# Kernel tuning notes

Hardware: AMD Instinct MI355X
Metric: run time of the kernel (lower is better)

The kernel has to match this reference:

```python
import jax, jax.numpy as jnp
import numpy as np

EMB = 300
H = 1024
V = 50004  # tgt_vocab_size + 4
B = 64
L = 1024


def setup_inputs() -> dict:
    key = jax.random.key(0)
    ks = jax.random.split(key, 16)
    s = 0.02
    return {
        "input": jax.random.randint(ks[0], (B,), 0, V),
        "hidden": jax.random.normal(ks[1], (1, B, H), jnp.float32),
        "source_hiddens": jax.random.normal(ks[2], (L, B, H), jnp.float32),
        "mask_src": jax.random.randint(ks[3], (B, L), 0, 2).astype(bool),
        "emb": jax.random.normal(ks[4], (V, EMB), jnp.float32) * s,
        "w_ih": jax.random.normal(ks[5], (3 * H, EMB), jnp.float32) * s,
        "w_hh": jax.random.normal(ks[6], (3 * H, H), jnp.float32) * s,
        "b_ih": jnp.zeros((3 * H,), jnp.float32),
        "b_hh": jnp.zeros((3 * H,), jnp.float32),
        "w_attn": jax.random.normal(ks[7], (H, H), jnp.float32) * s,
        "b_attn": jnp.zeros((H,), jnp.float32),
        "w_lin": jax.random.normal(ks[8], (H, 2 * H), jnp.float32) * s,
        "b_lin": jnp.zeros((H,), jnp.float32),
        "w_out": jax.random.normal(ks[9], (V, H), jnp.float32) * s,
        "b_out": jnp.zeros((V,), jnp.float32),
    }


def _decode_step(input, hidden, source_hiddens, mask_src, emb, w_ih, w_hh,
                 b_ih, b_hh, w_attn, b_attn, w_lin, b_lin, w_out, b_out):
    # Embedding lookup: [B, EMB]
    x = emb[input]
    h = hidden[0]  # [B, H]
    # GRU cell (PyTorch gate order: r, z, n)
    gi = x @ w_ih.T + b_ih          # [B, 3H]
    gh = h @ w_hh.T + b_hh          # [B, 3H]
    i_r, i_z, i_n = jnp.split(gi, 3, axis=-1)
    h_r, h_z, h_n = jnp.split(gh, 3, axis=-1)
    r = jax.nn.sigmoid(i_r + h_r)
    z = jax.nn.sigmoid(i_z + h_z)
    n = jnp.tanh(i_n + r * h_n)
    h_new = (1.0 - z) * n + z * h   # [B, H]

    # Bilinear attention over source: x_i' W y
    src = jnp.transpose(source_hiddens, (1, 0, 2))  # [B, L, H]
    Wy = h_new @ w_attn.T + b_attn                  # [B, H]
    xWy = jnp.einsum('blh,bh->bl', src, Wy)         # [B, L]
    xWy = jnp.where(mask_src, -jnp.inf, xWy)
    scores = jax.nn.softmax(xWy, axis=-1)           # [B, L]
    context = jnp.einsum('bl,blh->bh', scores, src) # [B, H]

    fused = jnp.tanh(jnp.concatenate([context, h_new], axis=1) @ w_lin.T + b_lin)
    logits = fused @ w_out.T + b_out                # [B, V]
    logp = jax.nn.log_softmax(logits, axis=1)
    return logp, h_new[None], scores


def reference(input, hidden, source_hiddens, mask_src, emb, w_ih, w_hh,
              b_ih, b_hh, w_attn, b_attn, w_lin, b_lin, w_out, b_out):
    return _decode_step(input, hidden, source_hiddens, mask_src, emb, w_ih,
                        w_hh, b_ih, b_hh, w_attn, b_attn, w_lin, b_lin,
                        w_out, b_out)
```

## Files before the change

### kernel.cpp

```cpp
#include <hip/hip_runtime.h>
#include <math.h>

#define EMB 300
#define HD  1024
#define VOC 50004
#define BB  64
#define LL  1024
#define NCH 16

typedef __attribute__((ext_vector_type(8))) short short8;
typedef __attribute__((ext_vector_type(4))) float f32x4;

#define WS_XT    0
#define WS_HT    (WS_XT + EMB*BB)
#define WS_HNT   (WS_HT + HD*BB)
#define WS_WYB   (WS_HNT + HD*BB)
#define WS_CTXT  (WS_WYB + HD*BB)
#define WS_AFR   (WS_CTXT + HD*BB)
#define WS_SRAW  (WS_AFR + HD*BB/2 + 64)
#define WS_MPART (WS_SRAW + BB*LL)
#define WS_DPART (WS_MPART + BB*NCH)
#define WS_CPART (WS_DPART + BB*NCH)
#define WS_LSE   (WS_CPART + BB*NCH*HD)

#define OFF_H ((size_t)BB*VOC)
#define OFF_S (OFF_H + (size_t)BB*HD)

__device__ __forceinline__ unsigned short f2bf(float f) {
  union { float f; unsigned u; } v; v.f = f;
  unsigned r = v.u + 0x7fffu + ((v.u >> 16) & 1u);
  return (unsigned short)(r >> 16);
}

__global__ __launch_bounds__(256) void k0_prep(
    const int* __restrict__ input, const float* __restrict__ hidden,
    const float* __restrict__ emb, float* __restrict__ ws)
{
  const int t = blockIdx.x * 256 + threadIdx.x;
  if (t < EMB * BB) {
    const int b = t & 63, k = t >> 6;
    ws[WS_XT + t] = emb[(size_t)input[b] * EMB + k];
  }
  const int u = t - EMB * BB;
  if (u >= 0 && u < HD * BB) {
    const int b = u & 63, k = u >> 6;
    ws[WS_HT + u] = hidden[(size_t)b * HD + k];
  }
}

__global__ __launch_bounds__(256) void k1_gru(
    const float* __restrict__ w_ih, const float* __restrict__ w_hh,
    const float* __restrict__ b_ih, const float* __restrict__ b_hh,
    float* __restrict__ ws, float* __restrict__ out)
{
  __shared__ float red[4][6][64];
  const int tid = threadIdx.x;
  const int b = tid & 63;
  const int w = tid >> 6;
  const int j = blockIdx.x;
  const float* xT = ws + WS_XT;
  const float* hT = ws + WS_HT;

  const float* wr = w_ih + (size_t)j * EMB;
  const float* wz = w_ih + (size_t)(HD + j) * EMB;
  const float* wn = w_ih + (size_t)(2 * HD + j) * EMB;
  float ar = 0.f, az = 0.f, an = 0.f;
  #pragma unroll 5
  for (int kk = 0; kk < 75; ++kk) {
    const int k = w * 75 + kk;
    const float x = xT[k * 64 + b];
    ar = fmaf(wr[k], x, ar); az = fmaf(wz[k], x, az); an = fmaf(wn[k], x, an);
  }
  const float4* vr4 = (const float4*)(w_hh + (size_t)j * HD);
  const float4* vz4 = (const float4*)(w_hh + (size_t)(HD + j) * HD);
  const float4* vn4 = (const float4*)(w_hh + (size_t)(2 * HD + j) * HD);
  float hr = 0.f, hz = 0.f, hn = 0.f;
  #pragma unroll 4
  for (int kk = 0; kk < 64; ++kk) {
    const float4 r4 = vr4[w * 64 + kk];
    const float4 z4 = vz4[w * 64 + kk];
    const float4 n4 = vn4[w * 64 + kk];
    const int kb = (w * 256 + kk * 4) * 64 + b;
    const float h0 = hT[kb], h1 = hT[kb + 64], h2 = hT[kb + 128], h3 = hT[kb + 192];
    hr = fmaf(r4.x, h0, hr); hr = fmaf(r4.y, h1, hr); hr = fmaf(r4.z, h2, hr); hr = fmaf(r4.w, h3, hr);
    hz = fmaf(z4.x, h0, hz); hz = fmaf(z4.y, h1, hz); hz = fmaf(z4.z, h2, hz); hz = fmaf(z4.w, h3, hz);
    hn = fmaf(n4.x, h0, hn); hn = fmaf(n4.y, h1, hn); hn = fmaf(n4.z, h2, hn); hn = fmaf(n4.w, h3, hn);
  }
  red[w][0][b] = ar; red[w][1][b] = az; red[w][2][b] = an;
  red[w][3][b] = hr; red[w][4][b] = hz; red[w][5][b] = hn;
  __syncthreads();
  if (w == 0) {
    float s[6];
    #pragma unroll
    for (int q = 0; q < 6; ++q)
      s[q] = red[0][q][b] + red[1][q][b] + red[2][q][b] + red[3][q][b];
    const float r = 1.f / (1.f + __expf(-(s[0] + b_ih[j] + s[3] + b_hh[j])));
    const float z = 1.f / (1.f + __expf(-(s[1] + b_ih[HD + j] + s[4] + b_hh[HD + j])));
    const float n = tanhf(s[2] + b_ih[2 * HD + j] + r * (s[5] + b_hh[2 * HD + j]));
    const float h_old = hT[j * 64 + b];
    const float hnew = (1.f - z) * n + z * h_old;
    ws[WS_HNT + j * 64 + b] = hnew;
    out[OFF_H + (size_t)b * HD + j] = hnew;
  }
}

__global__ __launch_bounds__(256) void k2_wy(
    const float* __restrict__ w_attn, const float* __restrict__ b_attn,
    float* __restrict__ ws)
{
  __shared__ float red[4][64];
  const int tid = threadIdx.x;
  const int b = tid & 63;
  const int w = tid >> 6;
  const int j = blockIdx.x;
  const float* hnT = ws + WS_HNT;
  const float4* w4 = (const float4*)(w_attn + (size_t)j * HD);
  float acc = 0.f;
  #pragma unroll 4
  for (int kk = 0; kk < 64; ++kk) {
    const float4 a4 = w4[w * 64 + kk];
    const int kb = (w * 256 + kk * 4) * 64 + b;
    acc = fmaf(a4.x, hnT[kb], acc);
    acc = fmaf(a4.y, hnT[kb + 64], acc);
    acc = fmaf(a4.z, hnT[kb + 128], acc);
    acc = fmaf(a4.w, hnT[kb + 192], acc);
  }
  red[w][b] = acc;
  __syncthreads();
  if (w == 0)
    ws[WS_WYB + (size_t)b * HD + j] = red[0][b] + red[1][b] + red[2][b] + red[3][b] + b_attn[j];
}

__global__ __launch_bounds__(256) void k3_attn(
    const float* __restrict__ src, const int* __restrict__ mask,
    float* __restrict__ ws)
{
  __shared__ float m_s[4], d_s[4];
  __shared__ float c_s[4 * 1024];
  const int tid = threadIdx.x;
  const int lane = tid & 63;
  const int wave = tid >> 6;
  const int b = blockIdx.y;
  const int chunk = blockIdx.x;

  float4 wy[4];
  const float4* wb4 = (const float4*)(ws + WS_WYB + (size_t)b * HD);
  #pragma unroll
  for (int q = 0; q < 4; ++q) wy[q] = wb4[q * 64 + lane];

  float4 c[4];
  #pragma unroll
  for (int q = 0; q < 4; ++q) { c[q].x = 0.f; c[q].y = 0.f; c[q].z = 0.f; c[q].w = 0.f; }
  float m_run = -INFINITY, d_run = 0.f;
  const int l0 = chunk * 64 + wave * 16;

  for (int i = 0; i < 16; ++i) {
    const int l = l0 + i;
    const float4* sp4 = (const float4*)(src + ((size_t)l * BB + b) * HD);
    float4 va[4];
    #pragma unroll
    for (int q = 0; q < 4; ++q) va[q] = sp4[q * 64 + lane];
    float s = 0.f;
    #pragma unroll
    for (int q = 0; q < 4; ++q) {
      s = fmaf(va[q].x, wy[q].x, s); s = fmaf(va[q].y, wy[q].y, s);
      s = fmaf(va[q].z, wy[q].z, s); s = fmaf(va[q].w, wy[q].w, s);
    }
    #pragma unroll
    for (int off = 32; off > 0; off >>= 1) s += __shfl_xor(s, off);

    const int msk = mask[(size_t)b * LL + l];
    if (lane == 0) ws[WS_SRAW + (size_t)b * LL + l] = msk ? -INFINITY : s;
    if (!msk) {
      if (s > m_run) {
        const float sc = __expf(m_run - s);
        m_run = s; d_run *= sc;
        #pragma unroll
        for (int q = 0; q < 4; ++q) {
          c[q].x *= sc; c[q].y *= sc; c[q].z *= sc; c[q].w *= sc;
        }
      }
      const float p = __expf(s - m_run);
      d_run += p;
      #pragma unroll
      for (int q = 0; q < 4; ++q) {
        c[q].x = fmaf(p, va[q].x, c[q].x); c[q].y = fmaf(p, va[q].y, c[q].y);
        c[q].z = fmaf(p, va[q].z, c[q].z); c[q].w = fmaf(p, va[q].w, c[q].w);
      }
    }
  }

  if (lane == 0) { m_s[wave] = m_run; d_s[wave] = d_run; }
  float4* cs4 = (float4*)c_s;
  #pragma unroll
  for (int q = 0; q < 4; ++q) cs4[wave * 256 + q * 64 + lane] = c[q];
  __syncthreads();

  float M = -INFINITY;
  #pragma unroll
  for (int w = 0; w < 4; ++w) if (d_s[w] > 0.f) M = fmaxf(M, m_s[w]);
  float e[4]; float D = 0.f;
  #pragma unroll
  for (int w = 0; w < 4; ++w) {
    e[w] = (d_s[w] > 0.f) ? __expf(m_s[w] - M) : 0.f;
    D += d_s[w] * e[w];
  }
  float4 a; a.x = a.y = a.z = a.w = 0.f;
  #pragma unroll
  for (int w = 0; w < 4; ++w) {
    const float4 cv = cs4[w * 256 + tid];
    a.x = fmaf(e[w], cv.x, a.x); a.y = fmaf(e[w], cv.y, a.y);
    a.z = fmaf(e[w], cv.z, a.z); a.w = fmaf(e[w], cv.w, a.w);
  }
  ((float4*)(ws + WS_CPART))[(size_t)(b * NCH + chunk) * 256 + tid] = a;
  if (tid == 0) {
    ws[WS_MPART + b * NCH + chunk] = M;
    ws[WS_DPART + b * NCH + chunk] = D;
  }
}

__global__ __launch_bounds__(256) void k3b_comb(
    float* __restrict__ ws, float* __restrict__ out)
{
  const int b = blockIdx.x;
  const int t = threadIdx.x;
  const float* mp = ws + WS_MPART + b * NCH;
  const float* dp = ws + WS_DPART + b * NCH;
  float M = -INFINITY;
  #pragma unroll
  for (int cc = 0; cc < NCH; ++cc) if (dp[cc] > 0.f) M = fmaxf(M, mp[cc]);
  float e[NCH]; float D = 0.f;
  #pragma unroll
  for (int cc = 0; cc < NCH; ++cc) {
    e[cc] = (dp[cc] > 0.f) ? __expf(mp[cc] - M) : 0.f;
    D += dp[cc] * e[cc];
  }
  const float invD = 1.f / D;
  const float4* cp4 = (const float4*)(ws + WS_CPART);
  float4 a; a.x = a.y = a.z = a.w = 0.f;
  #pragma unroll
  for (int cc = 0; cc < NCH; ++cc) {
    const float4 cv = cp4[(size_t)(b * NCH + cc) * 256 + t];
    a.x = fmaf(e[cc], cv.x, a.x); a.y = fmaf(e[cc], cv.y, a.y);
    a.z = fmaf(e[cc], cv.z, a.z); a.w = fmaf(e[cc], cv.w, a.w);
  }
  const int e0 = (t >> 6) * 256 + (t & 63) * 4;
  ws[WS_CTXT + (size_t)(e0 + 0) * 64 + b] = a.x * invD;
  ws[WS_CTXT + (size_t)(e0 + 1) * 64 + b] = a.y * invD;
  ws[WS_CTXT + (size_t)(e0 + 2) * 64 + b] = a.z * invD;
  ws[WS_CTXT + (size_t)(e0 + 3) * 64 + b] = a.w * invD;
  #pragma unroll
  for (int q = 0; q < 4; ++q) {
    const int l = t + 256 * q;
    const float s = ws[WS_SRAW + (size_t)b * LL + l];
    out[OFF_S + (size_t)b * LL + l] = __expf(s - M) * invD;
  }
}

__global__ __launch_bounds__(256) void k4_fused(
    const float* __restrict__ w_lin, const float* __restrict__ b_lin,
    float* __restrict__ ws)
{
  __shared__ float red[4][64];
  const int tid = threadIdx.x;
  const int b = tid & 63;
  const int w = tid >> 6;
  const int j = blockIdx.x;
  const float4* wl4 = (const float4*)(w_lin + (size_t)j * (2 * HD));
  const float* act = (w < 2) ? (ws + WS_CTXT) : (ws + WS_HNT);
  float acc = 0.f;
  #pragma unroll 4
  for (int kk = 0; kk < 128; ++kk) {
    const float4 a4 = wl4[w * 128 + kk];
    const int kb = ((w & 1) * 512 + kk * 4) * 64 + b;
    acc = fmaf(a4.x, act[kb], acc);
    acc = fmaf(a4.y, act[kb + 64], acc);
    acc = fmaf(a4.z, act[kb + 128], acc);
    acc = fmaf(a4.w, act[kb + 192], acc);
  }
  red[w][b] = acc;
  __syncthreads();
  if (w == 0) {
    const float f = tanhf(red[0][b] + red[1][b] + red[2][b] + red[3][b] + b_lin[j]);
    unsigned short* af = (unsigned short*)(ws + WS_AFR);
    const int t = j >> 5, kk = j & 31;
    const int lp = (b & 15) + 16 * (kk >> 3);
    const int mt = b >> 4;
    af[(((t * 4 + mt) * 64 + lp) << 3) + (kk & 7)] = f2bf(f);
  }
}

__global__ __launch_bounds__(256) void k5_logits(
    const float* __restrict__ w_out, const float* __restrict__ b_out,
    const float* __restrict__ ws, float* __restrict__ out)
{
  __shared__ unsigned short Bs[8 * 64 * 8];
  const int tid = threadIdx.x;
  const int lane = tid & 63;
  const int w = tid >> 6;
  const int vbase = blockIdx.x * 128;
  const unsigned short* af = (const unsigned short*)(ws + WS_AFR);

  f32x4 acc[4][2];
  #pragma unroll
  for (int mt = 0; mt < 4; ++mt)
    #pragma unroll
    for (int nb = 0; nb < 2; ++nb)
      acc[mt][nb] = (f32x4){0.f, 0.f, 0.f, 0.f};

  for (int t = 0; t < 32; ++t) {
    const int k0 = t * 32;
    __syncthreads();
    #pragma unroll
    for (int h = 0; h < 4; ++h) {
      const int idx = tid + 256 * h;
      const int vl = idx >> 3, s = idx & 7;
      int vg = vbase + vl; if (vg >= VOC) vg = VOC - 1;
      const float4 x = *(const float4*)(w_out + (size_t)vg * HD + k0 + s * 4);
      const int vt = vl >> 4;
      const int lp = (vl & 15) + 16 * (s >> 1);
      unsigned u0 = (unsigned)f2bf(x.x) | ((unsigned)f2bf(x.y) << 16);
      unsigned u1 = (unsigned)f2bf(x.z) | ((unsigned)f2bf(x.w) << 16);
      uint2* dst = (uint2*)&Bs[((vt * 64 + lp) << 3) + (s & 1) * 4];
      *dst = make_uint2(u0, u1);
    }
    __syncthreads();
    short8 a[4];
    #pragma unroll
    for (int mt = 0; mt < 4; ++mt)
      a[mt] = *(const short8*)(af + (((t * 4 + mt) * 64 + lane) << 3));
    short8 bf[2];
    #pragma unroll
    for (int nb = 0; nb < 2; ++nb)
      bf[nb] = *(const short8*)&Bs[(((w * 2 + nb) * 64 + lane)) << 3];
    #pragma unroll
    for (int mt = 0; mt < 4; ++mt)
      #pragma unroll
      for (int nb = 0; nb < 2; ++nb)
        acc[mt][nb] = __builtin_amdgcn_mfma_f32_16x16x32_bf16(a[mt], bf[nb], acc[mt][nb], 0, 0, 0);
  }

  #pragma unroll
  for (int nb = 0; nb < 2; ++nb) {
    const int v = vbase + (w * 2 + nb) * 16 + (lane & 15);
    if (v < VOC) {
      const float bias = b_out[v];
      #pragma unroll
      for (int mt = 0; mt < 4; ++mt) {
        #pragma unroll
        for (int r = 0; r < 4; ++r) {
          const int brow = mt * 16 + (lane >> 4) * 4 + r;
          out[(size_t)brow * VOC + v] = acc[mt][nb][r] + bias;
        }
      }
    }
  }
}

__global__ __launch_bounds__(256) void k6_lse(
    const float* __restrict__ out, float* __restrict__ ws)
{
  const int chunk = blockIdx.x, b = blockIdx.y, t = threadIdx.x;
  const int base = chunk * 12501;
  const float* row = out + (size_t)b * VOC;
  float m = -INFINITY, d = 0.f;
  for (int v = base + t; v < base + 12501; v += 256) {
    const float x = row[v];
    if (x > m) { d = d * __expf(m - x) + 1.f; m = x; }
    else d += __expf(x - m);
  }
  #pragma unroll
  for (int off = 32; off > 0; off >>= 1) {
    const float m2 = __shfl_xor(m, off);
    const float d2 = __shfl_xor(d, off);
    const float M = fmaxf(m, m2);
    d = d * __expf(m - M) + d2 * __expf(m2 - M);
    m = M;
  }
  __shared__ float ms[4], ds[4];
  if ((t & 63) == 0) { ms[t >> 6] = m; ds[t >> 6] = d; }
  __syncthreads();
  if (t == 0) {
    const float M = fmaxf(fmaxf(ms[0], ms[1]), fmaxf(ms[2], ms[3]));
    const float D = ds[0] * __expf(ms[0] - M) + ds[1] * __expf(ms[1] - M)
                  + ds[2] * __expf(ms[2] - M) + ds[3] * __expf(ms[3] - M);
    ws[WS_LSE + (b * 4 + chunk) * 2] = M;
    ws[WS_LSE + (b * 4 + chunk) * 2 + 1] = D;
  }
}

__global__ __launch_bounds__(256) void k7_sub(
    float* __restrict__ out, const float* __restrict__ ws)
{
  const int b = blockIdx.y;
  const int v = blockIdx.x * 256 + threadIdx.x;
  const float* p = ws + WS_LSE + b * 8;
  float M = fmaxf(fmaxf(p[0], p[2]), fmaxf(p[4], p[6]));
  float D = p[1] * __expf(p[0] - M) + p[3] * __expf(p[2] - M)
          + p[5] * __expf(p[4] - M) + p[7] * __expf(p[6] - M);
  const float lse = M + __logf(D);
  if (v < VOC) out[(size_t)b * VOC + v] -= lse;
}

extern "C" void kernel_launch(void* const* d_in, const int* in_sizes, int n_in,
                              void* d_out, int out_size, void* d_ws, size_t ws_size,
                              hipStream_t stream) {
  const int*   input  = (const int*)d_in[0];
  const float* hidden = (const float*)d_in[1];
  const float* src    = (const float*)d_in[2];
  const int*   mask   = (const int*)d_in[3];
  const float* emb    = (const float*)d_in[4];
  const float* w_ih   = (const float*)d_in[5];
  const float* w_hh   = (const float*)d_in[6];
  const float* b_ih   = (const float*)d_in[7];
  const float* b_hh   = (const float*)d_in[8];
  const float* w_attn = (const float*)d_in[9];
  const float* b_attn = (const float*)d_in[10];
  const float* w_lin  = (const float*)d_in[11];
  const float* b_lin  = (const float*)d_in[12];
  const float* w_out  = (const float*)d_in[13];
  const float* b_out  = (const float*)d_in[14];
  float* out = (float*)d_out;
  float* ws  = (float*)d_ws;

  k0_prep<<<331, 256, 0, stream>>>(input, hidden, emb, ws);
  k1_gru<<<1024, 256, 0, stream>>>(w_ih, w_hh, b_ih, b_hh, ws, out);
  k2_wy<<<1024, 256, 0, stream>>>(w_attn, b_attn, ws);
  k3_attn<<<dim3(NCH, BB), 256, 0, stream>>>(src, mask, ws);
  k3b_comb<<<BB, 256, 0, stream>>>(ws, out);
  k4_fused<<<1024, 256, 0, stream>>>(w_lin, b_lin, ws);
  k5_logits<<<(VOC + 127) / 128, 256, 0, stream>>>(w_out, b_out, ws, out);
  k6_lse<<<dim3(4, BB), 256, 0, stream>>>(out, ws);
  k7_sub<<<dim3((VOC + 255) / 256, BB), 256, 0, stream>>>(out, ws);
}
```

Measured before the change: 695.7 us.

## Stream w_out directly into MFMA registers with prefetch; vectorize log-softmax subtract

The logits kernel no longer stages converted w_out tiles through shared memory between barriers. Each lane now loads its own bf16 B-fragment straight from global memory, with one iteration of register prefetch. Blocks shrink to 64 vocab columns, and a launch-bounds occupancy hint is added. The final subtract kernel switches to float4 loads and stores. The aim is to remove LDS round trips and barrier stalls on this bandwidth-bound GEMM, at the cost of smaller per-block reuse and possibly less coalesced row-strided loads.

Result: no change. 704.2 us (+1.2%).

```diff
diff --git a/kernel.cpp b/kernel.cpp
--- a/kernel.cpp
+++ b/kernel.cpp
@@ -290,68 +290,70 @@
   }
 }
 
-__global__ __launch_bounds__(256) void k5_logits(
+__global__ __launch_bounds__(256, 4) void k5_logits(
     const float* __restrict__ w_out, const float* __restrict__ b_out,
     const float* __restrict__ ws, float* __restrict__ out)
 {
-  __shared__ unsigned short Bs[8 * 64 * 8];
   const int tid = threadIdx.x;
   const int lane = tid & 63;
   const int w = tid >> 6;
-  const int vbase = blockIdx.x * 128;
+  const int vbase = blockIdx.x * 64;
   const unsigned short* af = (const unsigned short*)(ws + WS_AFR);
 
-  f32x4 acc[4][2];
-  #pragma unroll
-  for (int mt = 0; mt < 4; ++mt)
-    #pragma unroll
-    for (int nb = 0; nb < 2; ++nb)
-      acc[mt][nb] = (f32x4){0.f, 0.f, 0.f, 0.f};
-
-  for (int t = 0; t < 32; ++t) {
-    const int k0 = t * 32;
-    __syncthreads();
-    #pragma unroll
-    for (int h = 0; h < 4; ++h) {
-      const int idx = tid + 256 * h;
-      const int vl = idx >> 3, s = idx & 7;
-      int vg = vbase + vl; if (vg >= VOC) vg = VOC - 1;
-      const float4 x = *(const float4*)(w_out + (size_t)vg * HD + k0 + s * 4);
-      const int vt = vl >> 4;
-      const int lp = (vl & 15) + 16 * (s >> 1);
-      unsigned u0 = (unsigned)f2bf(x.x) | ((unsigned)f2bf(x.y) << 16);
-      unsigned u1 = (unsigned)f2bf(x.z) | ((unsigned)f2bf(x.w) << 16);
-      uint2* dst = (uint2*)&Bs[((vt * 64 + lp) << 3) + (s & 1) * 4];
-      *dst = make_uint2(u0, u1);
-    }
-    __syncthreads();
-    short8 a[4];
-    #pragma unroll
-    for (int mt = 0; mt < 4; ++mt)
-      a[mt] = *(const short8*)(af + (((t * 4 + mt) * 64 + lane) << 3));
-    short8 bf[2];
-    #pragma unroll
-    for (int nb = 0; nb < 2; ++nb)
-      bf[nb] = *(const short8*)&Bs[(((w * 2 + nb) * 64 + lane)) << 3];
-    #pragma unroll
-    for (int mt = 0; mt < 4; ++mt)
+  const int v = vbase + w * 16 + (lane & 15);
+  const int vg = (v < VOC) ? v : (VOC - 1);
+  const float* wrow = w_out + (size_t)vg * HD + ((lane >> 4) << 3);
+
+  f32x4 acc[4];
+  #pragma unroll
+  for (int mt = 0; mt < 4; ++mt) acc[mt] = (f32x4){0.f, 0.f, 0.f, 0.f};
+
+  float4 c0 = *(const float4*)(wrow + 0);
+  float4 c1 = *(const float4*)(wrow + 4);
+  float4 c2 = *(const float4*)(wrow + 32);
+  float4 c3 = *(const float4*)(wrow + 36);
+
+  #pragma unroll 2
+  for (int t = 0; t < 16; ++t) {
+    float4 n0, n1, n2, n3;
+    if (t < 15) {
+      const float* p = wrow + (t + 1) * 64;
+      n0 = *(const float4*)(p + 0);
+      n1 = *(const float4*)(p + 4);
+      n2 = *(const float4*)(p + 32);
+      n3 = *(const float4*)(p + 36);
+    }
+    short8 b0, b1;
+    b0[0] = (short)f2bf(c0.x); b0[1] = (short)f2bf(c0.y);
+    b0[2] = (short)f2bf(c0.z); b0[3] = (short)f2bf(c0.w);
+    b0[4] = (short)f2bf(c1.x); b0[5] = (short)f2bf(c1.y);
+    b0[6] = (short)f2bf(c1.z); b0[7] = (short)f2bf(c1.w);
+    b1[0] = (short)f2bf(c2.x); b1[1] = (short)f2bf(c2.y);
+    b1[2] = (short)f2bf(c2.z); b1[3] = (short)f2bf(c2.w);
+    b1[4] = (short)f2bf(c3.x); b1[5] = (short)f2bf(c3.y);
+    b1[6] = (short)f2bf(c3.z); b1[7] = (short)f2bf(c3.w);
+
+    #pragma unroll
+    for (int mt = 0; mt < 4; ++mt) {
+      const short8 a0 = *(const short8*)(af + ((((t * 2 + 0) * 4 + mt) * 64 + lane) << 3));
+      acc[mt] = __builtin_amdgcn_mfma_f32_16x16x32_bf16(a0, b0, acc[mt], 0, 0, 0);
+    }
+    #pragma unroll
+    for (int mt = 0; mt < 4; ++mt) {
+      const short8 a1 = *(const short8*)(af + ((((t * 2 + 1) * 4 + mt) * 64 + lane) << 3));
+      acc[mt] = __builtin_amdgcn_mfma_f32_16x16x32_bf16(a1, b1, acc[mt], 0, 0, 0);
+    }
+    c0 = n0; c1 = n1; c2 = n2; c3 = n3;
+  }
+
+  if (v < VOC) {
+    const float bias = b_out[v];
+    #pragma unroll
+    for (int mt = 0; mt < 4; ++mt) {
       #pragma unroll
-      for (int nb = 0; nb < 2; ++nb)
-        acc[mt][nb] = __builtin_amdgcn_mfma_f32_16x16x32_bf16(a[mt], bf[nb], acc[mt][nb], 0, 0, 0);
-  }
-
-  #pragma unroll
-  for (int nb = 0; nb < 2; ++nb) {
-    const int v = vbase + (w * 2 + nb) * 16 + (lane & 15);
-    if (v < VOC) {
-      const float bias = b_out[v];
-      #pragma unroll
-      for (int mt = 0; mt < 4; ++mt) {
-        #pragma unroll
-        for (int r = 0; r < 4; ++r) {
-          const int brow = mt * 16 + (lane >> 4) * 4 + r;
-          out[(size_t)brow * VOC + v] = acc[mt][nb][r] + bias;
-        }
+      for (int r = 0; r < 4; ++r) {
+        const int brow = mt * 16 + ((lane >> 4) << 2) + r;
+        out[(size_t)brow * VOC + v] = acc[mt][r] + bias;
       }
     }
   }
@@ -393,13 +395,18 @@
     float* __restrict__ out, const float* __restrict__ ws)
 {
   const int b = blockIdx.y;
-  const int v = blockIdx.x * 256 + threadIdx.x;
+  const int i = blockIdx.x * 256 + threadIdx.x;
   const float* p = ws + WS_LSE + b * 8;
   float M = fmaxf(fmaxf(p[0], p[2]), fmaxf(p[4], p[6]));
   float D = p[1] * __expf(p[0] - M) + p[3] * __expf(p[2] - M)
           + p[5] * __expf(p[4] - M) + p[7] * __expf(p[6] - M);
   const float lse = M + __logf(D);
-  if (v < VOC) out[(size_t)b * VOC + v] -= lse;
+  if (i < 12501) {
+    float4* o = (float4*)(out + (size_t)b * VOC) + i;
+    float4 x = *o;
+    x.x -= lse; x.y -= lse; x.z -= lse; x.w -= lse;
+    *o = x;
+  }
 }
 
 extern "C" void kernel_launch(void* const* d_in, const int* in_sizes, int n_in,
@@ -429,7 +436,7 @@
   k3_attn<<<dim3(NCH, BB), 256, 0, stream>>>(src, mask, ws);
   k3b_comb<<<BB, 256, 0, stream>>>(ws, out);
   k4_fused<<<1024, 256, 0, stream>>>(w_lin, b_lin, ws);
-  k5_logits<<<(VOC + 127) / 128, 256, 0, stream>>>(w_out, b_out, ws, out);
+  k5_logits<<<(VOC + 63) / 64, 256, 0, stream>>>(w_out, b_out, ws, out);
   k6_lse<<<dim3(4, BB), 256, 0, stream>>>(out, ws);
-  k7_sub<<<dim3((VOC + 255) / 256, BB), 256, 0, stream>>>(out, ws);
-}
+  k7_sub<<<dim3(49, BB), 256, 0, stream>>>(out, ws);
+}
```
